# Performance work log

Measured on AMD Instinct MI355X. Metric: run time of the kernel, lower is better.

## Reference

```python
import jax, jax.numpy as jnp
import numpy as np

B, T, D = 4, 8192, 512
H = 8
DH = D // H  # per-head dim (dim_a // num_heads)

def _xavier(key, shape):
    fan_out, fan_in = shape
    std = np.sqrt(2.0 / (fan_in + fan_out))
    return jax.random.normal(key, shape, dtype=jnp.float32) * std

def setup_inputs() -> dict:
    key = jax.random.key(0)
    ks = jax.random.split(key, 7)
    return {
        'q': jax.random.normal(ks[0], (B, T, D), dtype=jnp.float32),
        'k': jax.random.normal(ks[1], (B, T, D), dtype=jnp.float32),
        'v': jax.random.normal(ks[2], (B, T, D), dtype=jnp.float32),
        'Wq': _xavier(ks[3], (D, D)), 'bq': jnp.zeros((D,), jnp.float32),
        'Wk': _xavier(ks[4], (D, D)), 'bk': jnp.zeros((D,), jnp.float32),
        'Wv': _xavier(ks[5], (D, D)), 'bv': jnp.zeros((D,), jnp.float32),
        'Wo': _xavier(ks[6], (D, D)), 'bo': jnp.zeros((D,), jnp.float32),
    }

def reference(q, k, v, Wq, bq, Wk, bk, Wv, bv, Wo, bo):
    # projections (nn.Linear: x @ W.T + b)
    qp = q @ Wq.T + bq  # [B,T,D]
    kp = k @ Wk.T + bk
    vp = v @ Wv.T + bv
    # split into heads: [B,T,H,DH]
    qh = (jax.nn.elu(qp) + 1.0).reshape(B, T, H, DH)
    kh = (jax.nn.elu(kp) + 1.0).reshape(B, T, H, DH)
    vh = vp.reshape(B, T, H, DH)
    # non-causal linear attention (mask=None path)
    context = jnp.einsum('bthc,bthd->bhcd', kh, vh)          # [B,H,DH,DH]
    numerator = jnp.einsum('bthc,bhcd->bthd', qh, context)    # [B,T,H,DH]
    denominator = jnp.einsum('bthc,bhc->bth', qh, kh.sum(axis=1))
    o = numerator / denominator[..., None]                    # [B,T,H,DH]
    o = o.reshape(B, T, D)
    return o @ Wo.T + bo
```

## Files before the change

### kernel.cpp

```cpp
#include <hip/hip_runtime.h>


typedef float v4f __attribute__((ext_vector_type(4)));
typedef short v8s __attribute__((ext_vector_type(8)));

__device__ __forceinline__ ushort f2bf(float f) {
  unsigned u = __float_as_uint(f);
  u += 0x7FFFu + ((u >> 16) & 1u);
  return (ushort)(u >> 16);
}
__device__ __forceinline__ float bf2f(ushort h) {
  return __uint_as_float(((unsigned)h) << 16);
}
__device__ __forceinline__ unsigned pk2(float a, float b) {
  return (unsigned)f2bf(a) | ((unsigned)f2bf(b) << 16);
}

__global__ __launch_bounds__(256) void proj_kernel(
    const float* __restrict__ X0, const float* __restrict__ X1, const float* __restrict__ X2,
    const float* __restrict__ W0, const float* __restrict__ W1, const float* __restrict__ W2,
    const float* __restrict__ Bb0, const float* __restrict__ Bb1, const float* __restrict__ Bb2,
    ushort* __restrict__ Y0, ushort* __restrict__ Y1, ushort* __restrict__ Y2) {
  __shared__ char As[16384];
  __shared__ char Bs[16384];
  const int z = blockIdx.z;
  const float* __restrict__ X  = (z == 0) ? X0  : (z == 1) ? X1  : X2;
  const float* __restrict__ W  = (z == 0) ? W0  : (z == 1) ? W1  : W2;
  const float* __restrict__ Bb = (z == 0) ? Bb0 : (z == 1) ? Bb1 : Bb2;
  ushort* __restrict__ Y       = (z == 0) ? Y0  : (z == 1) ? Y1  : Y2;
  const bool do_elu = (z < 2);

  const int tid = threadIdx.x;
  const int lane = tid & 63;
  const int wv = tid >> 6;
  const int wr = wv >> 1, wc = wv & 1;
  const int n0 = blockIdx.x * 128;
  const int m0 = blockIdx.y * 128;

  const v4f vzero = {0.f, 0.f, 0.f, 0.f};
  v4f acc[4][4];
#pragma unroll
  for (int i = 0; i < 4; ++i)
#pragma unroll
    for (int j = 0; j < 4; ++j) acc[i][j] = vzero;

  for (int k0 = 0; k0 < 512; k0 += 64) {
    __syncthreads();
#pragma unroll
    for (int r = 0; r < 8; ++r) {
      int s = tid + (r << 8);
      int row = s >> 4;
      int kq = (s & 15) << 2;
      v4f xv = *reinterpret_cast<const v4f*>(X + (size_t)(m0 + row) * 512 + k0 + kq);
      ushort4 hv = make_ushort4(f2bf(xv[0]), f2bf(xv[1]), f2bf(xv[2]), f2bf(xv[3]));
      int off = (row << 7) + (((kq >> 3) ^ (row & 7)) << 4) + ((kq & 7) << 1);
      *reinterpret_cast<ushort4*>(As + off) = hv;
    }
#pragma unroll
    for (int r = 0; r < 8; ++r) {
      int s = tid + (r << 8);
      int row = s >> 4;
      int kq = (s & 15) << 2;
      v4f wvv = *reinterpret_cast<const v4f*>(W + (size_t)(n0 + row) * 512 + k0 + kq);
      ushort4 hv = make_ushort4(f2bf(wvv[0]), f2bf(wvv[1]), f2bf(wvv[2]), f2bf(wvv[3]));
      int off = (row << 7) + (((kq >> 3) ^ (row & 7)) << 4) + ((kq & 7) << 1);
      *reinterpret_cast<ushort4*>(Bs + off) = hv;
    }
    __syncthreads();
#pragma unroll
    for (int kk = 0; kk < 2; ++kk) {
      const int kq = (kk << 5) + ((lane >> 4) << 3);
      const int kb = kq >> 3;
      v8s af[4], bfr[4];
#pragma unroll
      for (int mi = 0; mi < 4; ++mi) {
        int row = (wr << 6) + (mi << 4) + (lane & 15);
        af[mi] = *reinterpret_cast<const v8s*>(As + (row << 7) + ((kb ^ (row & 7)) << 4));
      }
#pragma unroll
      for (int ni = 0; ni < 4; ++ni) {
        int col = (wc << 6) + (ni << 4) + (lane & 15);
        bfr[ni] = *reinterpret_cast<const v8s*>(Bs + (col << 7) + ((kb ^ (col & 7)) << 4));
      }
#pragma unroll
      for (int mi = 0; mi < 4; ++mi)
#pragma unroll
        for (int ni = 0; ni < 4; ++ni)
          acc[mi][ni] = __builtin_amdgcn_mfma_f32_16x16x32_bf16(af[mi], bfr[ni], acc[mi][ni], 0, 0, 0);
    }
  }

#pragma unroll
  for (int ni = 0; ni < 4; ++ni) {
    const int col = n0 + (wc << 6) + (ni << 4) + (lane & 15);
    const float bv = Bb[col];
#pragma unroll
    for (int mi = 0; mi < 4; ++mi) {
#pragma unroll
      for (int j = 0; j < 4; ++j) {
        int row = m0 + (wr << 6) + (mi << 4) + ((lane >> 4) << 2) + j;
        float zv = acc[mi][ni][j] + bv;
        float val = do_elu ? ((zv > 0.f) ? (zv + 1.f) : __expf(zv)) : zv;
        Y[(size_t)row * 512 + col] = f2bf(val);
      }
    }
  }
}

__global__ __launch_bounds__(256) void ctx_kernel(
    const ushort* __restrict__ KH, const ushort* __restrict__ VH,
    float* __restrict__ CTX, float* __restrict__ KSUM) {
  __shared__ ushort kl[4096];
  __shared__ ushort vl[4096];
  const int tid = threadIdx.x;
  const int bh = blockIdx.y;
  const int b = bh >> 3, h = bh & 7;
  const int t0 = blockIdx.x << 9;
  const int c0 = (tid >> 4) << 2;
  const int d0 = (tid & 15) << 2;
  float acc[4][4];
#pragma unroll
  for (int i = 0; i < 4; ++i)
#pragma unroll
    for (int j = 0; j < 4; ++j) acc[i][j] = 0.f;
  float ks = 0.f;

  for (int sub = 0; sub < 8; ++sub) {
    __syncthreads();
#pragma unroll
    for (int r = 0; r < 2; ++r) {
      int s = tid + (r << 8);
      int row = s >> 3;
      int cb = (s & 7) << 3;
      size_t src = ((size_t)(b * 8192 + t0 + (sub << 6) + row)) * 512 + (h << 6) + cb;
      *reinterpret_cast<uint4*>(&kl[(row << 6) + cb]) = *reinterpret_cast<const uint4*>(KH + src);
      *reinterpret_cast<uint4*>(&vl[(row << 6) + cb]) = *reinterpret_cast<const uint4*>(VH + src);
    }
    __syncthreads();
#pragma unroll 4
    for (int t = 0; t < 64; ++t) {
      ushort4 kv = *reinterpret_cast<const ushort4*>(&kl[(t << 6) + c0]);
      ushort4 vv = *reinterpret_cast<const ushort4*>(&vl[(t << 6) + d0]);
      float ka[4] = {bf2f(kv.x), bf2f(kv.y), bf2f(kv.z), bf2f(kv.w)};
      float va[4] = {bf2f(vv.x), bf2f(vv.y), bf2f(vv.z), bf2f(vv.w)};
#pragma unroll
      for (int i = 0; i < 4; ++i)
#pragma unroll
        for (int j = 0; j < 4; ++j) acc[i][j] += ka[i] * va[j];
    }
    if (tid < 64) {
#pragma unroll 8
      for (int t = 0; t < 64; ++t) ks += bf2f(kl[(t << 6) + tid]);
    }
  }
#pragma unroll
  for (int i = 0; i < 4; ++i)
#pragma unroll
    for (int j = 0; j < 4; ++j)
      atomicAdd(&CTX[(bh << 12) + ((c0 + i) << 6) + (d0 + j)], acc[i][j]);
  if (tid < 64) atomicAdd(&KSUM[(bh << 6) + tid], ks);
}

__global__ __launch_bounds__(256) void numdiv_kernel(
    const ushort* __restrict__ QH, const float* __restrict__ CTX,
    const float* __restrict__ KSUM, ushort* __restrict__ O) {
  __shared__ float ctxl[4096];
  __shared__ float ksl[64];
  __shared__ ushort qtl[64 * 138];
  const int tid = threadIdx.x;
  const int bh = blockIdx.y;
  const int b = bh >> 3, h = bh & 7;
  const int t0 = blockIdx.x << 7;

#pragma unroll
  for (int r = 0; r < 4; ++r) {
    int s = tid + (r << 8);
    int row = s >> 4;
    int c4 = (s & 15) << 2;
    *reinterpret_cast<v4f*>(&ctxl[(row << 6) + c4]) =
        *reinterpret_cast<const v4f*>(&CTX[(bh << 12) + (row << 6) + c4]);
  }
  if (tid < 64) ksl[tid] = KSUM[(bh << 6) + tid];
#pragma unroll
  for (int r = 0; r < 4; ++r) {
    int s = tid + (r << 8);
    int trow = s >> 3;
    int cb = (s & 7) << 3;
    uint4 raw = *reinterpret_cast<const uint4*>(
        QH + ((size_t)(b * 8192 + t0 + trow)) * 512 + (h << 6) + cb);
    const ushort* p = reinterpret_cast<const ushort*>(&raw);
#pragma unroll
    for (int i = 0; i < 8; ++i) qtl[(cb + i) * 138 + trow] = p[i];
  }
  __syncthreads();

  const int l = tid & 63;
  const int dw = (tid >> 6) << 4;
  float a0[16], a1[16];
#pragma unroll
  for (int j = 0; j < 16; ++j) { a0[j] = 0.f; a1[j] = 0.f; }
  float den0 = 0.f, den1 = 0.f;

  for (int c = 0; c < 64; ++c) {
    float q0 = bf2f(qtl[c * 138 + l]);
    float q1 = bf2f(qtl[c * 138 + 64 + l]);
    float kv = ksl[c];
    den0 += q0 * kv;
    den1 += q1 * kv;
#pragma unroll
    for (int p4 = 0; p4 < 4; ++p4) {
      v4f cv = *reinterpret_cast<const v4f*>(&ctxl[(c << 6) + dw + (p4 << 2)]);
#pragma unroll
      for (int jj = 0; jj < 4; ++jj) {
        a0[(p4 << 2) + jj] += q0 * cv[jj];
        a1[(p4 << 2) + jj] += q1 * cv[jj];
      }
    }
  }
  float i0 = 1.f / den0, i1 = 1.f / den1;
  {
    size_t ro = ((size_t)(b * 8192 + t0 + l)) * 512 + (h << 6) + dw;
    uint4 w0 = make_uint4(pk2(a0[0] * i0, a0[1] * i0), pk2(a0[2] * i0, a0[3] * i0),
                          pk2(a0[4] * i0, a0[5] * i0), pk2(a0[6] * i0, a0[7] * i0));
    uint4 w1 = make_uint4(pk2(a0[8] * i0, a0[9] * i0), pk2(a0[10] * i0, a0[11] * i0),
                          pk2(a0[12] * i0, a0[13] * i0), pk2(a0[14] * i0, a0[15] * i0));
    *reinterpret_cast<uint4*>(O + ro) = w0;
    *reinterpret_cast<uint4*>(O + ro + 8) = w1;
  }
  {
    size_t ro = ((size_t)(b * 8192 + t0 + 64 + l)) * 512 + (h << 6) + dw;
    uint4 w0 = make_uint4(pk2(a1[0] * i1, a1[1] * i1), pk2(a1[2] * i1, a1[3] * i1),
                          pk2(a1[4] * i1, a1[5] * i1), pk2(a1[6] * i1, a1[7] * i1));
    uint4 w1 = make_uint4(pk2(a1[8] * i1, a1[9] * i1), pk2(a1[10] * i1, a1[11] * i1),
                          pk2(a1[12] * i1, a1[13] * i1), pk2(a1[14] * i1, a1[15] * i1));
    *reinterpret_cast<uint4*>(O + ro) = w0;
    *reinterpret_cast<uint4*>(O + ro + 8) = w1;
  }
}

__global__ __launch_bounds__(256) void out_kernel(
    const ushort* __restrict__ O, const float* __restrict__ Wo,
    const float* __restrict__ bo, float* __restrict__ OUT) {
  __shared__ char As[16384];
  __shared__ char Bs[16384];
  const int tid = threadIdx.x;
  const int lane = tid & 63;
  const int wv = tid >> 6;
  const int wr = wv >> 1, wc = wv & 1;
  const int n0 = blockIdx.x * 128;
  const int m0 = blockIdx.y * 128;

  const v4f vzero = {0.f, 0.f, 0.f, 0.f};
  v4f acc[4][4];
#pragma unroll
  for (int i = 0; i < 4; ++i)
#pragma unroll
    for (int j = 0; j < 4; ++j) acc[i][j] = vzero;

  for (int k0 = 0; k0 < 512; k0 += 64) {
    __syncthreads();
#pragma unroll
    for (int r = 0; r < 4; ++r) {
      int s = tid + (r << 8);
      int row = s >> 3;
      int kc = (s & 7) << 3;
      uint4 raw = *reinterpret_cast<const uint4*>(O + (size_t)(m0 + row) * 512 + k0 + kc);
      int off = (row << 7) + (((kc >> 3) ^ (row & 7)) << 4);
      *reinterpret_cast<uint4*>(As + off) = raw;
    }
#pragma unroll
    for (int r = 0; r < 8; ++r) {
      int s = tid + (r << 8);
      int row = s >> 4;
      int kq = (s & 15) << 2;
      v4f wvv = *reinterpret_cast<const v4f*>(Wo + (size_t)(n0 + row) * 512 + k0 + kq);
      ushort4 hv = make_ushort4(f2bf(wvv[0]), f2bf(wvv[1]), f2bf(wvv[2]), f2bf(wvv[3]));
      int off = (row << 7) + (((kq >> 3) ^ (row & 7)) << 4) + ((kq & 7) << 1);
      *reinterpret_cast<ushort4*>(Bs + off) = hv;
    }
    __syncthreads();
#pragma unroll
    for (int kk = 0; kk < 2; ++kk) {
      const int kq = (kk << 5) + ((lane >> 4) << 3);
      const int kb = kq >> 3;
      v8s af[4], bfr[4];
#pragma unroll
      for (int mi = 0; mi < 4; ++mi) {
        int row = (wr << 6) + (mi << 4) + (lane & 15);
        af[mi] = *reinterpret_cast<const v8s*>(As + (row << 7) + ((kb ^ (row & 7)) << 4));
      }
#pragma unroll
      for (int ni = 0; ni < 4; ++ni) {
        int col = (wc << 6) + (ni << 4) + (lane & 15);
        bfr[ni] = *reinterpret_cast<const v8s*>(Bs + (col << 7) + ((kb ^ (col & 7)) << 4));
      }
#pragma unroll
      for (int mi = 0; mi < 4; ++mi)
#pragma unroll
        for (int ni = 0; ni < 4; ++ni)
          acc[mi][ni] = __builtin_amdgcn_mfma_f32_16x16x32_bf16(af[mi], bfr[ni], acc[mi][ni], 0, 0, 0);
    }
  }

#pragma unroll
  for (int ni = 0; ni < 4; ++ni) {
    const int col = n0 + (wc << 6) + (ni << 4) + (lane & 15);
    const float bv = bo[col];
#pragma unroll
    for (int mi = 0; mi < 4; ++mi) {
#pragma unroll
      for (int j = 0; j < 4; ++j) {
        int row = m0 + (wr << 6) + (mi << 4) + ((lane >> 4) << 2) + j;
        OUT[(size_t)row * 512 + col] = acc[mi][ni][j] + bv;
      }
    }
  }
}

extern "C" void kernel_launch(void* const* d_in, const int* in_sizes, int n_in,
                              void* d_out, int out_size, void* d_ws, size_t ws_size,
                              hipStream_t stream) {
  const float* q  = (const float*)d_in[0];
  const float* k  = (const float*)d_in[1];
  const float* v  = (const float*)d_in[2];
  const float* Wq = (const float*)d_in[3];
  const float* bq = (const float*)d_in[4];
  const float* Wk = (const float*)d_in[5];
  const float* bk = (const float*)d_in[6];
  const float* Wv = (const float*)d_in[7];
  const float* bv = (const float*)d_in[8];
  const float* Wo = (const float*)d_in[9];
  const float* bo = (const float*)d_in[10];
  float* out = (float*)d_out;

  char* ws = (char*)d_ws;
  const size_t SZ = 32768ull * 512ull * 2ull;
  ushort* qh = (ushort*)(ws);
  ushort* kh = (ushort*)(ws + SZ);
  ushort* vh = (ushort*)(ws + 2 * SZ);
  ushort* o  = qh;
  float* ctx  = (float*)(ws + 3 * SZ);
  float* ksum = (float*)(ws + 3 * SZ + 524288);

  hipMemsetAsync(ws + 3 * SZ, 0, 524288 + 8192, stream);

  proj_kernel<<<dim3(4, 256, 3), 256, 0, stream>>>(q, k, v, Wq, Wk, Wv, bq, bk, bv, qh, kh, vh);
  ctx_kernel<<<dim3(16, 32), 256, 0, stream>>>(kh, vh, ctx, ksum);
  numdiv_kernel<<<dim3(64, 32), 256, 0, stream>>>(qh, ctx, ksum, o);
  out_kernel<<<dim3(4, 256), 256, 0, stream>>>(o, Wo, bo, out);
}
```

Measured before the change: 479.9 us.

## Pre-convert weights to bf16, widen GEMM tiles, use MFMA for context reduction

A new prep kernel converts all four weight matrices to bf16 once, in a padded, k-sliced layout. The projection and output GEMMs then load that layout straight into LDS with global_load_lds. These GEMMs now run 512-thread blocks that each cover all 512 output columns for 128 rows, so every X row is read and converted only once instead of once per column tile. The context kernel replaces its scalar FMA outer product with bf16 MFMA on transposed K/V tiles and reduces partial results across waves in LDS before the atomics. The intent is to cut redundant fp32 weight and activation traffic and per-tile conversion work, at the cost of an extra launch, larger LDS use and lower occupancy.

```diff
diff --git a/kernel.cpp b/kernel.cpp
--- a/kernel.cpp
+++ b/kernel.cpp
@@ -3,6 +3,13 @@
 
 typedef float v4f __attribute__((ext_vector_type(4)));
 typedef short v8s __attribute__((ext_vector_type(8)));
+
+typedef __attribute__((address_space(3))) unsigned int as3_u32;
+typedef __attribute__((address_space(1))) unsigned int as1_u32;
+
+__device__ __forceinline__ void glds16(const void* g, void* l) {
+  __builtin_amdgcn_global_load_lds((const as1_u32*)g, (as3_u32*)l, 16, 0, 0);
+}
 
 __device__ __forceinline__ ushort f2bf(float f) {
   unsigned u = __float_as_uint(f);
@@ -16,93 +23,115 @@
   return (unsigned)f2bf(a) | ((unsigned)f2bf(b) << 16);
 }
 
-__global__ __launch_bounds__(256) void proj_kernel(
+__global__ __launch_bounds__(256) void prep_kernel(
+    const float* __restrict__ Wq, const float* __restrict__ Wk,
+    const float* __restrict__ Wv, const float* __restrict__ Wo,
+    char* __restrict__ Wsw) {
+  int s = blockIdx.x * 256 + threadIdx.x;
+  int m = s >> 15;
+  int r = s & 32767;
+  int n = r >> 6;
+  int ks = (r >> 2) & 15;
+  int kb = r & 3;
+  const float* W = (m == 0) ? Wq : (m == 1) ? Wk : (m == 2) ? Wv : Wo;
+  const float* src = W + (size_t)n * 512 + ks * 32 + kb * 8;
+  v4f a = *reinterpret_cast<const v4f*>(src);
+  v4f c = *reinterpret_cast<const v4f*>(src + 4);
+  uint4 hv = make_uint4(pk2(a[0], a[1]), pk2(a[2], a[3]), pk2(c[0], c[1]), pk2(c[2], c[3]));
+  *reinterpret_cast<uint4*>(Wsw + (size_t)m * 655360 + ks * 40960 + n * 80 + kb * 16) = hv;
+}
+
+__global__ __launch_bounds__(512, 6) void proj_kernel(
     const float* __restrict__ X0, const float* __restrict__ X1, const float* __restrict__ X2,
-    const float* __restrict__ W0, const float* __restrict__ W1, const float* __restrict__ W2,
+    const char* __restrict__ WswBase,
     const float* __restrict__ Bb0, const float* __restrict__ Bb1, const float* __restrict__ Bb2,
     ushort* __restrict__ Y0, ushort* __restrict__ Y1, ushort* __restrict__ Y2) {
-  __shared__ char As[16384];
-  __shared__ char Bs[16384];
-  const int z = blockIdx.z;
+  __shared__ char As[128 * 80];
+  __shared__ char Bs[512 * 80];
+  const int z = blockIdx.y;
   const float* __restrict__ X  = (z == 0) ? X0  : (z == 1) ? X1  : X2;
-  const float* __restrict__ W  = (z == 0) ? W0  : (z == 1) ? W1  : W2;
   const float* __restrict__ Bb = (z == 0) ? Bb0 : (z == 1) ? Bb1 : Bb2;
   ushort* __restrict__ Y       = (z == 0) ? Y0  : (z == 1) ? Y1  : Y2;
+  const char* __restrict__ Wsw = WswBase + (size_t)z * 655360;
   const bool do_elu = (z < 2);
 
   const int tid = threadIdx.x;
   const int lane = tid & 63;
   const int wv = tid >> 6;
-  const int wr = wv >> 1, wc = wv & 1;
-  const int n0 = blockIdx.x * 128;
-  const int m0 = blockIdx.y * 128;
+  const int wr = wv >> 2, wc = wv & 3;
+  const int m0 = blockIdx.x * 128;
+
+  const int arow = tid >> 2;
+  const int ac4 = (tid & 3) << 2;
+  const float* xrow = X + (size_t)(m0 + arow) * 512 + ac4;
 
   const v4f vzero = {0.f, 0.f, 0.f, 0.f};
-  v4f acc[4][4];
+  v4f acc[4][8];
 #pragma unroll
   for (int i = 0; i < 4; ++i)
 #pragma unroll
-    for (int j = 0; j < 4; ++j) acc[i][j] = vzero;
-
-  for (int k0 = 0; k0 < 512; k0 += 64) {
-    __syncthreads();
-#pragma unroll
-    for (int r = 0; r < 8; ++r) {
-      int s = tid + (r << 8);
-      int row = s >> 4;
-      int kq = (s & 15) << 2;
-      v4f xv = *reinterpret_cast<const v4f*>(X + (size_t)(m0 + row) * 512 + k0 + kq);
-      ushort4 hv = make_ushort4(f2bf(xv[0]), f2bf(xv[1]), f2bf(xv[2]), f2bf(xv[3]));
-      int off = (row << 7) + (((kq >> 3) ^ (row & 7)) << 4) + ((kq & 7) << 1);
-      *reinterpret_cast<ushort4*>(As + off) = hv;
-    }
-#pragma unroll
-    for (int r = 0; r < 8; ++r) {
-      int s = tid + (r << 8);
-      int row = s >> 4;
-      int kq = (s & 15) << 2;
-      v4f wvv = *reinterpret_cast<const v4f*>(W + (size_t)(n0 + row) * 512 + k0 + kq);
-      ushort4 hv = make_ushort4(f2bf(wvv[0]), f2bf(wvv[1]), f2bf(wvv[2]), f2bf(wvv[3]));
-      int off = (row << 7) + (((kq >> 3) ^ (row & 7)) << 4) + ((kq & 7) << 1);
-      *reinterpret_cast<ushort4*>(Bs + off) = hv;
-    }
-    __syncthreads();
-#pragma unroll
-    for (int kk = 0; kk < 2; ++kk) {
-      const int kq = (kk << 5) + ((lane >> 4) << 3);
-      const int kb = kq >> 3;
-      v8s af[4], bfr[4];
-#pragma unroll
-      for (int mi = 0; mi < 4; ++mi) {
-        int row = (wr << 6) + (mi << 4) + (lane & 15);
-        af[mi] = *reinterpret_cast<const v8s*>(As + (row << 7) + ((kb ^ (row & 7)) << 4));
+    for (int j = 0; j < 8; ++j) acc[i][j] = vzero;
+
+  for (int ks = 0; ks < 16; ++ks) {
+    const int k0 = ks << 5;
+    __syncthreads();
+    {
+      const char* wsrc = Wsw + ks * 40960 + wv * 1024 + lane * 16;
+      char* bdst = Bs + wv * 1024;
+#pragma unroll
+      for (int i = 0; i < 5; ++i) glds16(wsrc + i * 8192, bdst + i * 8192);
+    }
+#pragma unroll
+    for (int j = 0; j < 2; ++j) {
+      v4f xv = *reinterpret_cast<const v4f*>(xrow + k0 + j * 16);
+      uint2 hv;
+      hv.x = pk2(xv[0], xv[1]);
+      hv.y = pk2(xv[2], xv[3]);
+      int kk = ac4 + (j << 4);
+      *reinterpret_cast<uint2*>(As + arow * 80 + ((kk >> 3) << 4) + ((ac4 & 7) << 1)) = hv;
+    }
+    __syncthreads();
+
+    const int ko = (lane >> 4) << 4;
+    v8s bfrg[8], afrg[4];
+#pragma unroll
+    for (int ni = 0; ni < 8; ++ni) {
+      int col = (wc << 7) + (ni << 4) + (lane & 15);
+      bfrg[ni] = *reinterpret_cast<const v8s*>(Bs + col * 80 + ko);
+    }
+#pragma unroll
+    for (int mi = 0; mi < 4; ++mi) {
+      int row = (wr << 6) + (mi << 4) + (lane & 15);
+      afrg[mi] = *reinterpret_cast<const v8s*>(As + row * 80 + ko);
+    }
+#pragma unroll
+    for (int mi = 0; mi < 4; ++mi)
+#pragma unroll
+      for (int ni = 0; ni < 8; ++ni)
+        acc[mi][ni] = __builtin_amdgcn_mfma_f32_16x16x32_bf16(bfrg[ni], afrg[mi], acc[mi][ni], 0, 0, 0);
+  }
+
+#pragma unroll
+  for (int ni = 0; ni < 8; ++ni) {
+    const int col4 = (wc << 7) + (ni << 4) + ((lane >> 4) << 2);
+    v4f bb = *reinterpret_cast<const v4f*>(Bb + col4);
+#pragma unroll
+    for (int mi = 0; mi < 4; ++mi) {
+      const int row = m0 + (wr << 6) + (mi << 4) + (lane & 15);
+      float v0 = acc[mi][ni][0] + bb[0];
+      float v1 = acc[mi][ni][1] + bb[1];
+      float v2 = acc[mi][ni][2] + bb[2];
+      float v3 = acc[mi][ni][3] + bb[3];
+      if (do_elu) {
+        v0 = (v0 > 0.f) ? (v0 + 1.f) : __expf(v0);
+        v1 = (v1 > 0.f) ? (v1 + 1.f) : __expf(v1);
+        v2 = (v2 > 0.f) ? (v2 + 1.f) : __expf(v2);
+        v3 = (v3 > 0.f) ? (v3 + 1.f) : __expf(v3);
       }
-#pragma unroll
-      for (int ni = 0; ni < 4; ++ni) {
-        int col = (wc << 6) + (ni << 4) + (lane & 15);
-        bfr[ni] = *reinterpret_cast<const v8s*>(Bs + (col << 7) + ((kb ^ (col & 7)) << 4));
-      }
-#pragma unroll
-      for (int mi = 0; mi < 4; ++mi)
-#pragma unroll
-        for (int ni = 0; ni < 4; ++ni)
-          acc[mi][ni] = __builtin_amdgcn_mfma_f32_16x16x32_bf16(af[mi], bfr[ni], acc[mi][ni], 0, 0, 0);
-    }
-  }
-
-#pragma unroll
-  for (int ni = 0; ni < 4; ++ni) {
-    const int col = n0 + (wc << 6) + (ni << 4) + (lane & 15);
-    const float bv = Bb[col];
-#pragma unroll
-    for (int mi = 0; mi < 4; ++mi) {
-#pragma unroll
-      for (int j = 0; j < 4; ++j) {
-        int row = m0 + (wr << 6) + (mi << 4) + ((lane >> 4) << 2) + j;
-        float zv = acc[mi][ni][j] + bv;
-        float val = do_elu ? ((zv > 0.f) ? (zv + 1.f) : __expf(zv)) : zv;
-        Y[(size_t)row * 512 + col] = f2bf(val);
-      }
+      uint2 o;
+      o.x = pk2(v0, v1);
+      o.y = pk2(v2, v3);
+      *reinterpret_cast<uint2*>(Y + (size_t)row * 512 + col4) = o;
     }
   }
 }
@@ -110,55 +139,141 @@
 __global__ __launch_bounds__(256) void ctx_kernel(
     const ushort* __restrict__ KH, const ushort* __restrict__ VH,
     float* __restrict__ CTX, float* __restrict__ KSUM) {
-  __shared__ ushort kl[4096];
-  __shared__ ushort vl[4096];
+  __shared__ char sm[34816];
+  __shared__ float ksp[256];
+  ushort* klT = (ushort*)sm;
+  ushort* vlT = (ushort*)(sm + 17408);
+  float* red0 = (float*)sm;
+  float* red1 = (float*)(sm + 16384);
+
   const int tid = threadIdx.x;
+  const int lane = tid & 63;
+  const int wv = tid >> 6;
   const int bh = blockIdx.y;
   const int b = bh >> 3, h = bh & 7;
-  const int t0 = blockIdx.x << 9;
-  const int c0 = (tid >> 4) << 2;
-  const int d0 = (tid & 15) << 2;
-  float acc[4][4];
+  const int tbase = blockIdx.x << 10;
+
+  const v4f vzero = {0.f, 0.f, 0.f, 0.f};
+  v4f acc[4][4];
 #pragma unroll
   for (int i = 0; i < 4; ++i)
 #pragma unroll
-    for (int j = 0; j < 4; ++j) acc[i][j] = 0.f;
+    for (int j = 0; j < 4; ++j) acc[i][j] = vzero;
   float ks = 0.f;
 
-  for (int sub = 0; sub < 8; ++sub) {
+  const int c8 = (tid & 7) << 3;
+  const int tp = (tid >> 3) << 1;
+
+  for (int it = 0; it < 8; ++it) {
     __syncthreads();
 #pragma unroll
     for (int r = 0; r < 2; ++r) {
-      int s = tid + (r << 8);
-      int row = s >> 3;
-      int cb = (s & 7) << 3;
-      size_t src = ((size_t)(b * 8192 + t0 + (sub << 6) + row)) * 512 + (h << 6) + cb;
-      *reinterpret_cast<uint4*>(&kl[(row << 6) + cb]) = *reinterpret_cast<const uint4*>(KH + src);
-      *reinterpret_cast<uint4*>(&vl[(row << 6) + cb]) = *reinterpret_cast<const uint4*>(VH + src);
-    }
-    __syncthreads();
-#pragma unroll 4
-    for (int t = 0; t < 64; ++t) {
-      ushort4 kv = *reinterpret_cast<const ushort4*>(&kl[(t << 6) + c0]);
-      ushort4 vv = *reinterpret_cast<const ushort4*>(&vl[(t << 6) + d0]);
-      float ka[4] = {bf2f(kv.x), bf2f(kv.y), bf2f(kv.z), bf2f(kv.w)};
-      float va[4] = {bf2f(vv.x), bf2f(vv.y), bf2f(vv.z), bf2f(vv.w)};
-#pragma unroll
-      for (int i = 0; i < 4; ++i)
-#pragma unroll
-        for (int j = 0; j < 4; ++j) acc[i][j] += ka[i] * va[j];
-    }
-    if (tid < 64) {
-#pragma unroll 8
-      for (int t = 0; t < 64; ++t) ks += bf2f(kl[(t << 6) + tid]);
-    }
-  }
-#pragma unroll
-  for (int i = 0; i < 4; ++i)
-#pragma unroll
-    for (int j = 0; j < 4; ++j)
-      atomicAdd(&CTX[(bh << 12) + ((c0 + i) << 6) + (d0 + j)], acc[i][j]);
-  if (tid < 64) atomicAdd(&KSUM[(bh << 6) + tid], ks);
+      int tloc = tp + (r << 6);
+      size_t g = ((size_t)(b * 8192 + tbase + (it << 7) + tloc)) * 512 + (h << 6) + c8;
+      uint4 ka = *reinterpret_cast<const uint4*>(KH + g);
+      uint4 kb = *reinterpret_cast<const uint4*>(KH + g + 512);
+      uint4 va = *reinterpret_cast<const uint4*>(VH + g);
+      uint4 vb = *reinterpret_cast<const uint4*>(VH + g + 512);
+      const ushort* pka = (const ushort*)&ka;
+      const ushort* pkb = (const ushort*)&kb;
+      const ushort* pva = (const ushort*)&va;
+      const ushort* pvb = (const ushort*)&vb;
+#pragma unroll
+      for (int i = 0; i < 8; ++i) {
+        unsigned kw = (unsigned)pka[i] | ((unsigned)pkb[i] << 16);
+        unsigned vw = (unsigned)pva[i] | ((unsigned)pvb[i] << 16);
+        *reinterpret_cast<unsigned*>((char*)klT + (c8 + i) * 272 + tloc * 2) = kw;
+        *reinterpret_cast<unsigned*>((char*)vlT + (c8 + i) * 272 + tloc * 2) = vw;
+      }
+    }
+    __syncthreads();
+    const int tw = wv << 5;
+    const int ko = (tw + ((lane >> 4) << 3)) << 1;
+    v8s af[4], bf_[4];
+#pragma unroll
+    for (int ci = 0; ci < 4; ++ci)
+      af[ci] = *reinterpret_cast<const v8s*>((char*)klT + ((ci << 4) + (lane & 15)) * 272 + ko);
+#pragma unroll
+    for (int di = 0; di < 4; ++di)
+      bf_[di] = *reinterpret_cast<const v8s*>((char*)vlT + ((di << 4) + (lane & 15)) * 272 + ko);
+#pragma unroll
+    for (int ci = 0; ci < 4; ++ci)
+#pragma unroll
+      for (int di = 0; di < 4; ++di)
+        acc[ci][di] = __builtin_amdgcn_mfma_f32_16x16x32_bf16(af[ci], bf_[di], acc[ci][di], 0, 0, 0);
+#pragma unroll
+    for (int q = 0; q < 4; ++q) {
+      v8s kv = *reinterpret_cast<const v8s*>((char*)klT + lane * 272 + ((tw + (q << 3)) << 1));
+#pragma unroll
+      for (int i = 0; i < 8; ++i) ks += bf2f((ushort)kv[i]);
+    }
+  }
+
+  __syncthreads();
+  if (wv == 2) {
+#pragma unroll
+    for (int ci = 0; ci < 4; ++ci)
+#pragma unroll
+      for (int di = 0; di < 4; ++di)
+#pragma unroll
+        for (int j = 0; j < 4; ++j)
+          red0[((ci << 4) + ((lane >> 4) << 2) + j) * 64 + (di << 4) + (lane & 15)] = acc[ci][di][j];
+  }
+  if (wv == 3) {
+#pragma unroll
+    for (int ci = 0; ci < 4; ++ci)
+#pragma unroll
+      for (int di = 0; di < 4; ++di)
+#pragma unroll
+        for (int j = 0; j < 4; ++j)
+          red1[((ci << 4) + ((lane >> 4) << 2) + j) * 64 + (di << 4) + (lane & 15)] = acc[ci][di][j];
+  }
+  ksp[tid] = ks;
+  __syncthreads();
+  if (wv == 0) {
+#pragma unroll
+    for (int ci = 0; ci < 4; ++ci)
+#pragma unroll
+      for (int di = 0; di < 4; ++di)
+#pragma unroll
+        for (int j = 0; j < 4; ++j)
+          acc[ci][di][j] += red0[((ci << 4) + ((lane >> 4) << 2) + j) * 64 + (di << 4) + (lane & 15)];
+  }
+  if (wv == 1) {
+#pragma unroll
+    for (int ci = 0; ci < 4; ++ci)
+#pragma unroll
+      for (int di = 0; di < 4; ++di)
+#pragma unroll
+        for (int j = 0; j < 4; ++j)
+          acc[ci][di][j] += red1[((ci << 4) + ((lane >> 4) << 2) + j) * 64 + (di << 4) + (lane & 15)];
+  }
+  __syncthreads();
+  if (wv == 1) {
+#pragma unroll
+    for (int ci = 0; ci < 4; ++ci)
+#pragma unroll
+      for (int di = 0; di < 4; ++di)
+#pragma unroll
+        for (int j = 0; j < 4; ++j)
+          red0[((ci << 4) + ((lane >> 4) << 2) + j) * 64 + (di << 4) + (lane & 15)] = acc[ci][di][j];
+  }
+  __syncthreads();
+  if (wv == 0) {
+#pragma unroll
+    for (int ci = 0; ci < 4; ++ci)
+#pragma unroll
+      for (int di = 0; di < 4; ++di)
+#pragma unroll
+        for (int j = 0; j < 4; ++j) {
+          int c = (ci << 4) + ((lane >> 4) << 2) + j;
+          int d = (di << 4) + (lane & 15);
+          float val = acc[ci][di][j] + red0[c * 64 + d];
+          atomicAdd(&CTX[(bh << 12) + (c << 6) + d], val);
+        }
+    float ksv = ksp[lane] + ksp[64 + lane] + ksp[128 + lane] + ksp[192 + lane];
+    atomicAdd(&KSUM[(bh << 6) + lane], ksv);
+  }
 }
 
 __global__ __launch_bounds__(256) void numdiv_kernel(
@@ -238,81 +353,73 @@
   }
 }
 
-__global__ __launch_bounds__(256) void out_kernel(
-    const ushort* __restrict__ O, const float* __restrict__ Wo,
+__global__ __launch_bounds__(512, 6) void out_kernel(
+    const ushort* __restrict__ O, const char* __restrict__ WswO,
     const float* __restrict__ bo, float* __restrict__ OUT) {
-  __shared__ char As[16384];
-  __shared__ char Bs[16384];
+  __shared__ char As[128 * 80];
+  __shared__ char Bs[512 * 80];
   const int tid = threadIdx.x;
   const int lane = tid & 63;
   const int wv = tid >> 6;
-  const int wr = wv >> 1, wc = wv & 1;
-  const int n0 = blockIdx.x * 128;
-  const int m0 = blockIdx.y * 128;
+  const int wr = wv >> 2, wc = wv & 3;
+  const int m0 = blockIdx.x * 128;
+
+  const int arow = tid >> 2;
+  const int ak = tid & 3;
 
   const v4f vzero = {0.f, 0.f, 0.f, 0.f};
-  v4f acc[4][4];
+  v4f acc[4][8];
 #pragma unroll
   for (int i = 0; i < 4; ++i)
 #pragma unroll
-    for (int j = 0; j < 4; ++j) acc[i][j] = vzero;
-
-  for (int k0 = 0; k0 < 512; k0 += 64) {
-    __syncthreads();
-#pragma unroll
-    for (int r = 0; r < 4; ++r) {
-      int s = tid + (r << 8);
-      int row = s >> 3;
-      int kc = (s & 7) << 3;
-      uint4 raw = *reinterpret_cast<const uint4*>(O + (size_t)(m0 + row) * 512 + k0 + kc);
-      int off = (row << 7) + (((kc >> 3) ^ (row & 7)) << 4);
-      *reinterpret_cast<uint4*>(As + off) = raw;
-    }
-#pragma unroll
-    for (int r = 0; r < 8; ++r) {
-      int s = tid + (r << 8);
-      int row = s >> 4;
-      int kq = (s & 15) << 2;
-      v4f wvv = *reinterpret_cast<const v4f*>(Wo + (size_t)(n0 + row) * 512 + k0 + kq);
-      ushort4 hv = make_ushort4(f2bf(wvv[0]), f2bf(wvv[1]), f2bf(wvv[2]), f2bf(wvv[3]));
-      int off = (row << 7) + (((kq >> 3) ^ (row & 7)) << 4) + ((kq & 7) << 1);
-      *reinterpret_cast<ushort4*>(Bs + off) = hv;
-    }
-    __syncthreads();
-#pragma unroll
-    for (int kk = 0; kk < 2; ++kk) {
-      const int kq = (kk << 5) + ((lane >> 4) << 3);
-      const int kb = kq >> 3;
-      v8s af[4], bfr[4];
-#pragma unroll
-      for (int mi = 0; mi < 4; ++mi) {
-        int row = (wr << 6) + (mi << 4) + (lane & 15);
-        af[mi] = *reinterpret_cast<const v8s*>(As + (row << 7) + ((kb ^ (row & 7)) << 4));
-      }
-#pragma unroll
-      for (int ni = 0; ni < 4; ++ni) {
-        int col = (wc << 6) + (ni << 4) + (lane & 15);
-        bfr[ni] = *reinterpret_cast<const v8s*>(Bs + (col << 7) + ((kb ^ (col & 7)) << 4));
-      }
-#pragma unroll
-      for (int mi = 0; mi < 4; ++mi)
-#pragma unroll
-        for (int ni = 0; ni < 4; ++ni)
-          acc[mi][ni] = __builtin_amdgcn_mfma_f32_16x16x32_bf16(af[mi], bfr[ni], acc[mi][ni], 0, 0, 0);
-    }
-  }
-
-#pragma unroll
-  for (int ni = 0; ni < 4; ++ni) {
-    const int col = n0 + (wc << 6) + (ni << 4) + (lane & 15);
-    const float bv = bo[col];
+    for (int j = 0; j < 8; ++j) acc[i][j] = vzero;
+
+  for (int ks = 0; ks < 16; ++ks) {
+    __syncthreads();
+    {
+      const char* wsrc = WswO + ks * 40960 + wv * 1024 + lane * 16;
+      char* bdst = Bs + wv * 1024;
+#pragma unroll
+      for (int i = 0; i < 5; ++i) glds16(wsrc + i * 8192, bdst + i * 8192);
+    }
+    {
+      uint4 raw = *reinterpret_cast<const uint4*>(O + (size_t)(m0 + arow) * 512 + (ks << 5) + (ak << 3));
+      *reinterpret_cast<uint4*>(As + arow * 80 + (ak << 4)) = raw;
+    }
+    __syncthreads();
+
+    const int ko = (lane >> 4) << 4;
+    v8s bfrg[8], afrg[4];
+#pragma unroll
+    for (int ni = 0; ni < 8; ++ni) {
+      int col = (wc << 7) + (ni << 4) + (lane & 15);
+      bfrg[ni] = *reinterpret_cast<const v8s*>(Bs + col * 80 + ko);
+    }
 #pragma unroll
     for (int mi = 0; mi < 4; ++mi) {
-#pragma unroll
-      for (int j = 0; j < 4; ++j) {
-        int row = m0 + (wr << 6) + (mi << 4) + ((lane >> 4) << 2) + j;
-        OUT[(size_t)row * 512 + col] = acc[mi][ni][j] + bv;
-      }
+      int row = (wr << 6) + (mi << 4) + (lane & 15);
+      afrg[mi] = *reinterpret_cast<const v8s*>(As + row * 80 + ko);
+    }
+#pragma unroll
+    for (int mi = 0; mi < 4; ++mi)
+#pragma unroll
+      for (int ni = 0; ni < 8; ++ni)
+        acc[mi][ni] = __builtin_amdgcn_mfma_f32_16x16x32_bf16(bfrg[ni], afrg[mi], acc[mi][ni], 0, 0, 0);
+  }
+
+#pragma unroll
+  for (int ni = 0; ni < 8; ++ni) {
+    const int col4 = (wc << 7) + (ni << 4) + ((lane >> 4) << 2);
+    v4f bb = *reinterpret_cast<const v4f*>(bo + col4);
+#pragma unroll
+    for (int mi = 0; mi < 4; ++mi) {
+      const int row = m0 + (wr << 6) + (mi << 4) + (lane & 15);
+      v4f st;
+      st[0] = acc[mi][ni][0] + bb[0];
+      st[1] = acc[mi][ni][1] + bb[1];
+      st[2] = acc[mi][ni][2] + bb[2];
+      st[3] = acc[mi][ni][3] + bb[3];
+      *reinterpret_cast<v4f*>(OUT + (size_t)row * 512 + col4) = st;
     }
   }
 }
@@ -334,18 +441,18 @@
   float* out = (float*)d_out;
 
   char* ws = (char*)d_ws;
-  const size_t SZ = 32768ull * 512ull * 2ull;
+  const size_t SZ = 33554432ull;
   ushort* qh = (ushort*)(ws);
   ushort* kh = (ushort*)(ws + SZ);
   ushort* vh = (ushort*)(ws + 2 * SZ);
-  ushort* o  = qh;
   float* ctx  = (float*)(ws + 3 * SZ);
   float* ksum = (float*)(ws + 3 * SZ + 524288);
-
-  hipMemsetAsync(ws + 3 * SZ, 0, 524288 + 8192, stream);
-
-  proj_kernel<<<dim3(4, 256, 3), 256, 0, stream>>>(q, k, v, Wq, Wk, Wv, bq, bk, bv, qh, kh, vh);
-  ctx_kernel<<<dim3(16, 32), 256, 0, stream>>>(kh, vh, ctx, ksum);
-  numdiv_kernel<<<dim3(64, 32), 256, 0, stream>>>(qh, ctx, ksum, o);
-  out_kernel<<<dim3(4, 256), 256, 0, stream>>>(o, Wo, bo, out);
-}
+  char* wsw   = ws + 3 * SZ + 532480;
+
+  hipMemsetAsync(ws + 3 * SZ, 0, 532480, stream);
+  prep_kernel<<<512, 256, 0, stream>>>(Wq, Wk, Wv, Wo, wsw);
+  proj_kernel<<<dim3(256, 3), 512, 0, stream>>>(q, k, v, wsw, bq, bk, bv, qh, kh, vh);
+  ctx_kernel<<<dim3(8, 32), 256, 0, stream>>>(kh, vh, ctx, ksum);
+  numdiv_kernel<<<dim3(64, 32), 256, 0, stream>>>(qh, ctx, ksum, qh);
+  out_kernel<<<dim3(256), 512, 0, stream>>>(qh, wsw + 3 * 655360, bo, out);
+}
```

New measurement: 1.420 ms. 196% more time.
